# Kernel tuning notes

Measured on AMD Instinct MI355X. Metric: run time of the kernel, lower is better.

Reference implementation:

```python
import jax, jax.numpy as jnp
import numpy as np

K_NEIGHBORS = 16


def knn_idx(x, k):
    # x: (bs, n, 3) -> (bs, n, k) indices of k nearest points (incl. self)
    sq = jnp.sum(x * x, axis=-1)                      # (bs, n)
    inner = jnp.einsum('bnd,bmd->bnm', x, x)          # (bs, n, n)
    dist = sq[:, :, None] - 2.0 * inner + sq[:, None, :]
    _, idx = jax.lax.top_k(-dist, k)
    return idx


def gather_neighbors(feat, idx):
    # feat: (bs, n, d), idx: (bs, n, k) -> (bs, n, k, d)
    bs = feat.shape[0]
    return feat[jnp.arange(bs)[:, None, None], idx]


def setup_inputs() -> dict:
    key = jax.random.key(0)
    ks = jax.random.split(key, 20)
    bs, n, emb, inner, ph, ah = 4, 2048, 128, 128, 64, 4 * 128
    s = lambda k, sh, fan: jax.random.normal(k, sh, jnp.float32) * (1.0 / np.sqrt(fan))
    return {
        'query': jax.random.normal(ks[0], (bs, n, emb), jnp.float32),
        'key': jax.random.normal(ks[1], (bs, n, emb), jnp.float32),
        'value': jax.random.normal(ks[2], (bs, n, emb), jnp.float32),
        'canonical': jax.random.normal(ks[3], (bs, n, 3), jnp.float32),
        'wq': s(ks[4], (emb, inner), emb),
        'wk': s(ks[5], (emb, inner), emb),
        'wv': s(ks[6], (emb, inner), emb),
        'wo': s(ks[7], (inner, emb), inner),
        'bo': jnp.zeros((emb,), jnp.float32),
        'p1': s(ks[8], (3, ph), 3),
        'pb1': jnp.zeros((ph,), jnp.float32),
        'p2': s(ks[9], (ph, inner), ph),
        'pb2': jnp.zeros((inner,), jnp.float32),
        'a1': s(ks[10], (inner, ah), inner),
        'ab1': jnp.zeros((ah,), jnp.float32),
        'a2': s(ks[11], (ah, inner), ah),
        'ab2': jnp.zeros((inner,), jnp.float32),
    }


def reference(query, key, value, canonical, wq, wk, wv, wo, bo,
              p1, pb1, p2, pb2, a1, ab1, a2, ab2):
    k_nb = K_NEIGHBORS
    q = query @ wq                                    # (bs, n, d)
    k = key @ wk
    v = value @ wv
    idx = knn_idx(canonical, k_nb)                    # (bs, n, k)

    pos_nn = gather_neighbors(canonical, idx)         # (bs, n, k, 3)
    rel_pos = pos_nn - canonical[:, :, None, :]
    rel_pos_emb = jax.nn.relu(rel_pos @ p1 + pb1) @ p2 + pb2  # (bs, n, k, d)

    q_nn = gather_neighbors(q, idx)
    k_nn = gather_neighbors(k, idx)
    v_nn = gather_neighbors(v, idx) + rel_pos_emb

    sim = jax.nn.relu((q_nn - k_nn + rel_pos_emb) @ a1 + ab1) @ a2 + ab2
    attn = jax.nn.softmax(sim, axis=-1)               # softmax over feature dim
    norm = jnp.maximum(jnp.linalg.norm(attn, axis=-2, keepdims=True), 1e-12)
    attn = attn / norm                                # L2-normalize over neighbors

    agg = jnp.einsum('bijd,bijd->bid', attn, v_nn)    # (bs, n, d)
    return agg @ wo + bo
```

## Files before the change

kernel.cpp:

```cpp
#include <hip/hip_runtime.h>
#include <stdint.h>

typedef unsigned short u16;
typedef unsigned int u32;
typedef unsigned long long u64;
typedef __attribute__((ext_vector_type(8))) short short8;
typedef __attribute__((ext_vector_type(4))) float f32x4;

#define BSZ 4
#define NPT 2048
#define EMB 128
#define PH  64
#define AH  512
#define KNB 16

__device__ __forceinline__ u16 f2bf(float f) {
  union { float f; u32 u; } v; v.f = f;
  u32 r = (v.u >> 16) & 1u;
  v.u += 0x7fffu + r;
  return (u16)(v.u >> 16);
}
__device__ __forceinline__ float bf2f(u16 x) {
  union { u32 u; float f; } v; v.u = ((u32)x) << 16; return v.f;
}

__global__ __launch_bounds__(256) void k_transpose(
    const float* wq, const float* wk, const float* wv, const float* p2,
    const float* a1, const float* a2, const float* wo,
    u16* wqT, u16* wkT, u16* wvT, u16* p2T, u16* a1T, u16* a2T, u16* woT) {
  const float* src; u16* dst; int K, Nn;
  switch (blockIdx.x) {
    case 0: src = wq; dst = wqT; K = 128; Nn = 128; break;
    case 1: src = wk; dst = wkT; K = 128; Nn = 128; break;
    case 2: src = wv; dst = wvT; K = 128; Nn = 128; break;
    case 3: src = p2; dst = p2T; K = 64;  Nn = 128; break;
    case 4: src = a1; dst = a1T; K = 128; Nn = 512; break;
    case 5: src = a2; dst = a2T; K = 512; Nn = 128; break;
    default: src = wo; dst = woT; K = 128; Nn = 128; break;
  }
  for (int n = threadIdx.x; n < Nn; n += 256) {
    for (int k0 = 0; k0 < K; k0 += 8) {
      short8 vv;
      #pragma unroll
      for (int t = 0; t < 8; ++t)
        vv[t] = (short)f2bf(src[(k0 + t) * Nn + n]);
      *(short8*)(dst + n * K + k0) = vv;
    }
  }
}

__device__ __forceinline__ u32 f2sort(float f) {
  union { float f; u32 u; } v; v.f = f;
  return v.u ^ ((v.u >> 31) ? 0xFFFFFFFFu : 0x80000000u);
}

__global__ __launch_bounds__(256) void k_knn(const float* __restrict__ can,
                                             int* __restrict__ idx_out) {
  __shared__ float dists[4][NPT];
  int b = blockIdx.x >> 8;
  int qblk = blockIdx.x & 255;
  const float* cb = can + (size_t)b * NPT * 3;
  int wave = threadIdx.x >> 6, lane = threadIdx.x & 63;
  float* dw = dists[wave];
  #pragma unroll 1
  for (int t = 0; t < 2; ++t) {
    int i = qblk * 8 + wave * 2 + t;
    float xi = cb[i * 3 + 0], yi = cb[i * 3 + 1], zi = cb[i * 3 + 2];
    float sqi = __fadd_rn(__fadd_rn(__fmul_rn(xi, xi), __fmul_rn(yi, yi)),
                          __fmul_rn(zi, zi));
    u64 lmin = ~0ull;
    #pragma unroll 4
    for (int c = 0; c < NPT / 64; ++c) {
      int j = c * 64 + lane;
      const float* pj = cb + j * 3;
      float xj = pj[0], yj = pj[1], zj = pj[2];
      float sqj = __fadd_rn(__fadd_rn(__fmul_rn(xj, xj), __fmul_rn(yj, yj)),
                            __fmul_rn(zj, zj));
      float nn = __fadd_rn(__fadd_rn(__fmul_rn(xi, xj), __fmul_rn(yi, yj)),
                           __fmul_rn(zi, zj));
      float dist = __fadd_rn(__fsub_rn(sqi, __fmul_rn(2.0f, nn)), sqj);
      dw[j] = dist;
      u64 key = (((u64)f2sort(dist)) << 32) | (u32)j;
      lmin = key < lmin ? key : lmin;
    }
    #pragma unroll 1
    for (int r = 0; r < KNB; ++r) {
      u64 g = lmin;
      #pragma unroll
      for (int off = 32; off > 0; off >>= 1) {
        u64 o = __shfl_xor(g, off);
        g = o < g ? o : g;
      }
      int jw = (int)(u32)(g & 0xffffffffull);
      if (lane == 0) idx_out[((size_t)b * NPT + i) * KNB + r] = jw;
      if ((jw & 63) == lane) {
        union { u32 u; float f; } inf; inf.u = 0x7f800000u;
        dw[jw] = inf.f;
        lmin = ~0ull;
        #pragma unroll
        for (int c = 0; c < NPT / 64; ++c) {
          int j = c * 64 + lane;
          u64 key = (((u64)f2sort(dw[j])) << 32) | (u32)j;
          lmin = key < lmin ? key : lmin;
        }
      }
    }
  }
}

__device__ __forceinline__ void qkv_gemm(const u16* At, const u16* wT,
                                         int colbase, int fm, int quad,
                                         f32x4 acc[2][4]) {
  #pragma unroll
  for (int tn = 0; tn < 2; ++tn)
    #pragma unroll
    for (int tm = 0; tm < 4; ++tm) acc[tn][tm] = (f32x4){0.f, 0.f, 0.f, 0.f};
  #pragma unroll
  for (int ks = 0; ks < 4; ++ks) {
    int k0 = ks * 32 + quad * 8;
    short8 bfr0 = *(const short8*)(wT + (colbase + fm) * 128 + k0);
    short8 bfr1 = *(const short8*)(wT + (colbase + 16 + fm) * 128 + k0);
    #pragma unroll
    for (int tm = 0; tm < 4; ++tm) {
      short8 afr = *(const short8*)(At + (tm * 16 + fm) * 136 + k0);
      acc[0][tm] = __builtin_amdgcn_mfma_f32_16x16x32_bf16(afr, bfr0, acc[0][tm], 0, 0, 0);
      acc[1][tm] = __builtin_amdgcn_mfma_f32_16x16x32_bf16(afr, bfr1, acc[1][tm], 0, 0, 0);
    }
  }
}

__device__ __forceinline__ void qkv_stage(u16* At, const float* src, int rbase, int tid) {
  #pragma unroll
  for (int rep = 0; rep < 4; ++rep) {
    int linear = tid + 256 * rep;
    int row = linear >> 4;
    int c16 = linear & 15;
    const float* sp = src + (size_t)(rbase + row) * 128 + c16 * 8;
    f32x4 a = *(const f32x4*)(sp);
    f32x4 b = *(const f32x4*)(sp + 4);
    short8 vv;
    vv[0] = (short)f2bf(a[0]); vv[1] = (short)f2bf(a[1]);
    vv[2] = (short)f2bf(a[2]); vv[3] = (short)f2bf(a[3]);
    vv[4] = (short)f2bf(b[0]); vv[5] = (short)f2bf(b[1]);
    vv[6] = (short)f2bf(b[2]); vv[7] = (short)f2bf(b[3]);
    *(short8*)(At + row * 136 + c16 * 8) = vv;
  }
}

__global__ __launch_bounds__(256) void k_qkv(
    const float* __restrict__ query, const float* __restrict__ key,
    const float* __restrict__ value,
    const u16* __restrict__ wqT, const u16* __restrict__ wkT,
    const u16* __restrict__ wvT,
    u32* __restrict__ pv_out) {
  __shared__ __align__(16) u16 At[64 * 136];
  int tid = threadIdx.x;
  int rbase = blockIdx.x * 64;
  int lane = tid & 63, wave = tid >> 6;
  int fm = lane & 15, quad = lane >> 4;
  int colbase = wave * 32;
  f32x4 accq[2][4], acck[2][4];

  qkv_stage(At, query, rbase, tid);
  __syncthreads();
  qkv_gemm(At, wqT, colbase, fm, quad, accq);
  __syncthreads();
  qkv_stage(At, key, rbase, tid);
  __syncthreads();
  qkv_gemm(At, wkT, colbase, fm, quad, acck);
  u32 qk2[4][4];
  #pragma unroll
  for (int tm = 0; tm < 4; ++tm)
    #pragma unroll
    for (int r = 0; r < 4; ++r)
      qk2[tm][r] = (u32)f2bf(accq[0][tm][r] - acck[0][tm][r]) |
                   (((u32)f2bf(accq[1][tm][r] - acck[1][tm][r])) << 16);
  __syncthreads();
  qkv_stage(At, value, rbase, tid);
  __syncthreads();
  qkv_gemm(At, wvT, colbase, fm, quad, accq);
  #pragma unroll
  for (int tn = 0; tn < 2; ++tn) {
    int col = colbase + tn * 16 + fm;
    #pragma unroll
    for (int tm = 0; tm < 4; ++tm)
      #pragma unroll
      for (int r = 0; r < 4; ++r) {
        int row = tm * 16 + quad * 4 + r;
        u32 qkb = tn == 0 ? (qk2[tm][r] & 0xffffu) : (qk2[tm][r] >> 16);
        u32 pack = qkb | (((u32)f2bf(accq[tn][tm][r])) << 16);
        pv_out[(size_t)(rbase + row) * 128 + col] = pack;
      }
  }
}

#define XT_LD 136

__global__ __launch_bounds__(256, 3) void k_attn(
    const float* __restrict__ can,
    const u32* __restrict__ pv_g,
    const int* __restrict__ idx_g,
    const float* __restrict__ p1, const float* __restrict__ pb1,
    const u16* __restrict__ p2T, const float* __restrict__ pb2,
    const u16* __restrict__ a1T, const float* __restrict__ ab1,
    const u16* __restrict__ a2T, const float* __restrict__ ab2,
    const u16* __restrict__ woT, const float* __restrict__ bo,
    float* __restrict__ out) {
  __shared__ __align__(16) char smem[39168];
  u16* Xt = (u16*)(smem);
  u16* Hs = (u16*)(smem + 17408);
  u16* R1 = (u16*)(smem + 17408);
  float* Red1 = (float*)(smem + 34816);
  float* Red2 = (float*)(smem + 35840);
  float* Agg = (float*)(smem + 36864);
  int* Idx = (int*)(smem + 38912);

  const int b = blockIdx.x >> 9;
  const int qbase = (blockIdx.x & 511) * 4;
  const int tid = threadIdx.x;
  const int lane = tid & 63, wave = tid >> 6;
  const int fm = lane & 15, quad = lane >> 4;
  const int colbase = wave * 32;

  if (tid < 64) Idx[tid] = idx_g[((size_t)b * NPT + qbase) * KNB + tid];
  __syncthreads();

  u32 pvld[2][4][4];
  #pragma unroll
  for (int tn = 0; tn < 2; ++tn) {
    int col = colbase + tn * 16 + fm;
    #pragma unroll
    for (int tm = 0; tm < 4; ++tm)
      #pragma unroll
      for (int r = 0; r < 4; ++r) {
        int row = tm * 16 + quad * 4 + r;
        int j = Idx[row];
        pvld[tn][tm][r] = pv_g[((size_t)b * NPT + j) * EMB + col];
      }
  }

  {
    int row = tid >> 2, part = tid & 3;
    int j = Idx[row];
    int qi = qbase + (row >> 4);
    const float* cb = can + (size_t)b * NPT * 3;
    float r0 = cb[j * 3 + 0] - cb[qi * 3 + 0];
    float r1 = cb[j * 3 + 1] - cb[qi * 3 + 1];
    float r2 = cb[j * 3 + 2] - cb[qi * 3 + 2];
    #pragma unroll
    for (int hp = 0; hp < 8; ++hp) {
      int cp = part + 4 * hp;
      u32 pack = 0;
      #pragma unroll
      for (int e = 0; e < 2; ++e) {
        int hh = cp * 2 + e;
        float s = r0 * p1[hh];
        s = fmaf(r1, p1[PH + hh], s);
        s = fmaf(r2, p1[2 * PH + hh], s);
        s += pb1[hh];
        s = fmaxf(s, 0.0f);
        pack |= ((u32)f2bf(s)) << (16 * e);
      }
      *(u32*)(R1 + row * 72 + cp * 2) = pack;
    }
  }
  __syncthreads();

  u32 vp[4][4];
  {
    f32x4 acc[2][4];
    #pragma unroll
    for (int tn = 0; tn < 2; ++tn)
      #pragma unroll
      for (int tm = 0; tm < 4; ++tm) acc[tn][tm] = (f32x4){0.f, 0.f, 0.f, 0.f};
    #pragma unroll
    for (int ks = 0; ks < 2; ++ks) {
      int k0 = ks * 32 + quad * 8;
      short8 bfr0 = *(const short8*)(p2T + (colbase + fm) * PH + k0);
      short8 bfr1 = *(const short8*)(p2T + (colbase + 16 + fm) * PH + k0);
      #pragma unroll
      for (int tm = 0; tm < 4; ++tm) {
        short8 afr = *(const short8*)(R1 + (tm * 16 + fm) * 72 + k0);
        acc[0][tm] = __builtin_amdgcn_mfma_f32_16x16x32_bf16(afr, bfr0, acc[0][tm], 0, 0, 0);
        acc[1][tm] = __builtin_amdgcn_mfma_f32_16x16x32_bf16(afr, bfr1, acc[1][tm], 0, 0, 0);
      }
    }
    #pragma unroll
    for (int tn = 0; tn < 2; ++tn) {
      int col = colbase + tn * 16 + fm;
      float pb2c = pb2[col];
      #pragma unroll
      for (int tm = 0; tm < 4; ++tm)
        #pragma unroll
        for (int r = 0; r < 4; ++r) {
          int row = tm * 16 + quad * 4 + r;
          float rpe = acc[tn][tm][r] + pb2c;
          u32 w = pvld[tn][tm][r];
          Xt[row * XT_LD + col] = f2bf(bf2f((u16)(w & 0xffffu)) + rpe);
          u32 vb = (u32)f2bf(bf2f((u16)(w >> 16)) + rpe);
          if (tn == 0) vp[tm][r] = vb; else vp[tm][r] |= vb << 16;
        }
    }
  }
  __syncthreads();

  f32x4 accS[2][4];
  #pragma unroll
  for (int tn = 0; tn < 2; ++tn)
    #pragma unroll
    for (int tm = 0; tm < 4; ++tm) accS[tn][tm] = (f32x4){0.f, 0.f, 0.f, 0.f};
  #pragma unroll 1
  for (int c = 0; c < 4; ++c) {
    f32x4 acc1[2][4];
    #pragma unroll
    for (int tn = 0; tn < 2; ++tn)
      #pragma unroll
      for (int tm = 0; tm < 4; ++tm) acc1[tn][tm] = (f32x4){0.f, 0.f, 0.f, 0.f};
    #pragma unroll
    for (int ks = 0; ks < 4; ++ks) {
      int k0 = ks * 32 + quad * 8;
      short8 bfr0 = *(const short8*)(a1T + (c * 128 + colbase + fm) * 128 + k0);
      short8 bfr1 = *(const short8*)(a1T + (c * 128 + colbase + 16 + fm) * 128 + k0);
      #pragma unroll
      for (int tm = 0; tm < 4; ++tm) {
        short8 afr = *(const short8*)(Xt + (tm * 16 + fm) * XT_LD + k0);
        acc1[0][tm] = __builtin_amdgcn_mfma_f32_16x16x32_bf16(afr, bfr0, acc1[0][tm], 0, 0, 0);
        acc1[1][tm] = __builtin_amdgcn_mfma_f32_16x16x32_bf16(afr, bfr1, acc1[1][tm], 0, 0, 0);
      }
    }
    #pragma unroll
    for (int tn = 0; tn < 2; ++tn) {
      int lcol = colbase + tn * 16 + fm;
      float ab1c = ab1[c * 128 + lcol];
      #pragma unroll
      for (int tm = 0; tm < 4; ++tm)
        #pragma unroll
        for (int r = 0; r < 4; ++r) {
          int row = tm * 16 + quad * 4 + r;
          Hs[row * XT_LD + lcol] = f2bf(fmaxf(acc1[tn][tm][r] + ab1c, 0.0f));
        }
    }
    __syncthreads();
    #pragma unroll
    for (int ks = 0; ks < 4; ++ks) {
      int k0 = ks * 32 + quad * 8;
      short8 bfr0 = *(const short8*)(a2T + (colbase + fm) * AH + c * 128 + k0);
      short8 bfr1 = *(const short8*)(a2T + (colbase + 16 + fm) * AH + c * 128 + k0);
      #pragma unroll
      for (int tm = 0; tm < 4; ++tm) {
        short8 afr = *(const short8*)(Hs + (tm * 16 + fm) * XT_LD + k0);
        accS[0][tm] = __builtin_amdgcn_mfma_f32_16x16x32_bf16(afr, bfr0, accS[0][tm], 0, 0, 0);
        accS[1][tm] = __builtin_amdgcn_mfma_f32_16x16x32_bf16(afr, bfr1, accS[1][tm], 0, 0, 0);
      }
    }
    __syncthreads();
  }

  {
    float ab2c0 = ab2[colbase + fm];
    float ab2c1 = ab2[colbase + 16 + fm];
    float rm[4][4];
    #pragma unroll
    for (int tm = 0; tm < 4; ++tm)
      #pragma unroll
      for (int r = 0; r < 4; ++r) {
        accS[0][tm][r] += ab2c0;
        accS[1][tm][r] += ab2c1;
        rm[tm][r] = fmaxf(accS[0][tm][r], accS[1][tm][r]);
      }
    #pragma unroll
    for (int off = 1; off <= 8; off <<= 1)
      #pragma unroll
      for (int tm = 0; tm < 4; ++tm)
        #pragma unroll
        for (int r = 0; r < 4; ++r)
          rm[tm][r] = fmaxf(rm[tm][r], __shfl_xor(rm[tm][r], off));
    if (fm == 0) {
      #pragma unroll
      for (int tm = 0; tm < 4; ++tm)
        #pragma unroll
        for (int r = 0; r < 4; ++r)
          Red1[wave * 64 + tm * 16 + quad * 4 + r] = rm[tm][r];
    }
    __syncthreads();
    #pragma unroll
    for (int tm = 0; tm < 4; ++tm)
      #pragma unroll
      for (int r = 0; r < 4; ++r) {
        int row = tm * 16 + quad * 4 + r;
        float m = fmaxf(fmaxf(Red1[row], Red1[64 + row]),
                        fmaxf(Red1[128 + row], Red1[192 + row]));
        float e0 = __expf(accS[0][tm][r] - m);
        float e1 = __expf(accS[1][tm][r] - m);
        accS[0][tm][r] = e0;
        accS[1][tm][r] = e1;
        rm[tm][r] = e0 + e1;
      }
    #pragma unroll
    for (int off = 1; off <= 8; off <<= 1)
      #pragma unroll
      for (int tm = 0; tm < 4; ++tm)
        #pragma unroll
        for (int r = 0; r < 4; ++r)
          rm[tm][r] += __shfl_xor(rm[tm][r], off);
    if (fm == 0) {
      #pragma unroll
      for (int tm = 0; tm < 4; ++tm)
        #pragma unroll
        for (int r = 0; r < 4; ++r)
          Red2[wave * 64 + tm * 16 + quad * 4 + r] = rm[tm][r];
    }
    __syncthreads();
    #pragma unroll
    for (int tm = 0; tm < 4; ++tm)
      #pragma unroll
      for (int r = 0; r < 4; ++r) {
        int row = tm * 16 + quad * 4 + r;
        float sum = (Red2[row] + Red2[64 + row]) +
                    (Red2[128 + row] + Red2[192 + row]);
        float inv = 1.0f / sum;
        accS[0][tm][r] *= inv;
        accS[1][tm][r] *= inv;
      }
  }

  #pragma unroll
  for (int tn = 0; tn < 2; ++tn)
    #pragma unroll
    for (int tm = 0; tm < 4; ++tm) {
      float ssq = 0.f, wav = 0.f;
      #pragma unroll
      for (int r = 0; r < 4; ++r) {
        float a = accS[tn][tm][r];
        u16 vb = (u16)(tn == 0 ? (vp[tm][r] & 0xffffu) : (vp[tm][r] >> 16));
        ssq = fmaf(a, a, ssq);
        wav = fmaf(a, bf2f(vb), wav);
      }
      ssq += __shfl_xor(ssq, 16); ssq += __shfl_xor(ssq, 32);
      wav += __shfl_xor(wav, 16); wav += __shfl_xor(wav, 32);
      if (quad == 0)
        Agg[tm * EMB + colbase + tn * 16 + fm] =
            wav / fmaxf(sqrtf(ssq), 1e-12f);
    }
  __syncthreads();

  {
    int d = tid & 127, qp = tid >> 7;
    float boc = bo[d];
    #pragma unroll
    for (int qi2 = 0; qi2 < 2; ++qi2) {
      int q = qp * 2 + qi2;
      float o = 0.f;
      #pragma unroll
      for (int k8 = 0; k8 < 16; ++k8) {
        short8 w8 = *(const short8*)(woT + d * 128 + k8 * 8);
        #pragma unroll
        for (int e = 0; e < 8; ++e)
          o = fmaf(Agg[q * EMB + k8 * 8 + e], bf2f((u16)w8[e]), o);
      }
      out[((size_t)b * NPT + qbase + q) * EMB + d] = o + boc;
    }
  }
}

extern "C" void kernel_launch(void* const* d_in, const int* in_sizes, int n_in,
                              void* d_out, int out_size, void* d_ws, size_t ws_size,
                              hipStream_t stream) {
  (void)in_sizes; (void)n_in; (void)out_size; (void)ws_size;
  const float* query = (const float*)d_in[0];
  const float* key_i = (const float*)d_in[1];
  const float* value = (const float*)d_in[2];
  const float* can   = (const float*)d_in[3];
  const float* wq  = (const float*)d_in[4];
  const float* wk  = (const float*)d_in[5];
  const float* wv  = (const float*)d_in[6];
  const float* wo  = (const float*)d_in[7];
  const float* bo  = (const float*)d_in[8];
  const float* p1  = (const float*)d_in[9];
  const float* pb1 = (const float*)d_in[10];
  const float* p2  = (const float*)d_in[11];
  const float* pb2 = (const float*)d_in[12];
  const float* a1  = (const float*)d_in[13];
  const float* ab1 = (const float*)d_in[14];
  const float* a2  = (const float*)d_in[15];
  const float* ab2 = (const float*)d_in[16];

  char* ws = (char*)d_ws;
  u32* pv_ws = (u32*)(ws + 0);
  int* idx_ws  = (int*)(ws + 8388608);
  u16* wqT = (u16*)(ws + 8912896);
  u16* wkT = (u16*)(ws + 8945664);
  u16* wvT = (u16*)(ws + 8978432);
  u16* p2T = (u16*)(ws + 9011200);
  u16* a1T = (u16*)(ws + 9027584);
  u16* a2T = (u16*)(ws + 9158656);
  u16* woT = (u16*)(ws + 9289728);
  float* out = (float*)d_out;

  k_transpose<<<dim3(7), dim3(256), 0, stream>>>(
      wq, wk, wv, p2, a1, a2, wo, wqT, wkT, wvT, p2T, a1T, a2T, woT);
  k_knn<<<dim3(1024), dim3(256), 0, stream>>>(can, idx_ws);
  k_qkv<<<dim3(128), dim3(256), 0, stream>>>(
      query, key_i, value, wqT, wkT, wvT, pv_ws);
  k_attn<<<dim3(2048), dim3(256), 0, stream>>>(
      can, pv_ws, idx_ws, p1, pb1, p2T, pb2, a1T, ab1, a2T, ab2,
      woT, bo, out);
}
```

Baseline: 319.1 us.

## Give each wave one query's neighbor rows so softmax and MLP need no block syncs

The attention kernel's MFMA work is repartitioned from a column split (each wave owning 32 of 128 feature columns across all 64 neighbor rows) to a row split (each wave owning the 16 neighbor rows of one query across all 128 columns). Softmax over the feature dimension then reduces within a wave using shuffles, so the shared-memory max/sum reduction buffers and most __syncthreads barriers in the MLP chunk loop are dropped. Each wave now reads all B-fragments of a1/a2/p2 instead of a quarter of them, which raises weight-load traffic from L1/L2, while A-fragment reuse per wave falls. Shared memory shrinks slightly.

```diff
diff --git a/kernel.cpp b/kernel.cpp
--- a/kernel.cpp
+++ b/kernel.cpp
@@ -206,43 +206,39 @@
     const u16* __restrict__ a2T, const float* __restrict__ ab2,
     const u16* __restrict__ woT, const float* __restrict__ bo,
     float* __restrict__ out) {
-  __shared__ __align__(16) char smem[39168];
+  __shared__ __align__(16) char smem[37120];
   u16* Xt = (u16*)(smem);
   u16* Hs = (u16*)(smem + 17408);
   u16* R1 = (u16*)(smem + 17408);
-  float* Red1 = (float*)(smem + 34816);
-  float* Red2 = (float*)(smem + 35840);
-  float* Agg = (float*)(smem + 36864);
-  int* Idx = (int*)(smem + 38912);
+  float* Agg = (float*)(smem + 34816);
+  int* Idx = (int*)(smem + 36864);
 
   const int b = blockIdx.x >> 9;
   const int qbase = (blockIdx.x & 511) * 4;
   const int tid = threadIdx.x;
-  const int lane = tid & 63, wave = tid >> 6;
+  const int lane = tid & 63, w = tid >> 6;
   const int fm = lane & 15, quad = lane >> 4;
-  const int colbase = wave * 32;
 
   if (tid < 64) Idx[tid] = idx_g[((size_t)b * NPT + qbase) * KNB + tid];
   __syncthreads();
 
-  u32 pvld[2][4][4];
-  #pragma unroll
-  for (int tn = 0; tn < 2; ++tn) {
-    int col = colbase + tn * 16 + fm;
-    #pragma unroll
-    for (int tm = 0; tm < 4; ++tm)
-      #pragma unroll
-      for (int r = 0; r < 4; ++r) {
-        int row = tm * 16 + quad * 4 + r;
-        int j = Idx[row];
-        pvld[tn][tm][r] = pv_g[((size_t)b * NPT + j) * EMB + col];
-      }
+  int jreg[4];
+  #pragma unroll
+  for (int r = 0; r < 4; ++r) jreg[r] = Idx[w * 16 + quad * 4 + r];
+
+  u32 pvld[8][4];
+  #pragma unroll
+  for (int tn = 0; tn < 8; ++tn) {
+    int col = tn * 16 + fm;
+    #pragma unroll
+    for (int r = 0; r < 4; ++r)
+      pvld[tn][r] = pv_g[((size_t)b * NPT + jreg[r]) * EMB + col];
   }
 
   {
-    int row = tid >> 2, part = tid & 3;
-    int j = Idx[row];
-    int qi = qbase + (row >> 4);
+    int lrow = lane >> 2, part = lane & 3;
+    int j = Idx[w * 16 + lrow];
+    int qi = qbase + w;
     const float* cb = can + (size_t)b * NPT * 3;
     float r0 = cb[j * 3 + 0] - cb[qi * 3 + 0];
     float r1 = cb[j * 3 + 1] - cb[qi * 3 + 1];
@@ -261,187 +257,142 @@
         s = fmaxf(s, 0.0f);
         pack |= ((u32)f2bf(s)) << (16 * e);
       }
-      *(u32*)(R1 + row * 72 + cp * 2) = pack;
-    }
-  }
-  __syncthreads();
+      *(u32*)(R1 + (w * 16 + lrow) * 72 + cp * 2) = pack;
+    }
+  }
 
   u32 vp[4][4];
   {
-    f32x4 acc[2][4];
-    #pragma unroll
-    for (int tn = 0; tn < 2; ++tn)
-      #pragma unroll
-      for (int tm = 0; tm < 4; ++tm) acc[tn][tm] = (f32x4){0.f, 0.f, 0.f, 0.f};
+    f32x4 acc[8];
+    #pragma unroll
+    for (int tn = 0; tn < 8; ++tn) acc[tn] = (f32x4){0.f, 0.f, 0.f, 0.f};
     #pragma unroll
     for (int ks = 0; ks < 2; ++ks) {
       int k0 = ks * 32 + quad * 8;
-      short8 bfr0 = *(const short8*)(p2T + (colbase + fm) * PH + k0);
-      short8 bfr1 = *(const short8*)(p2T + (colbase + 16 + fm) * PH + k0);
-      #pragma unroll
-      for (int tm = 0; tm < 4; ++tm) {
-        short8 afr = *(const short8*)(R1 + (tm * 16 + fm) * 72 + k0);
-        acc[0][tm] = __builtin_amdgcn_mfma_f32_16x16x32_bf16(afr, bfr0, acc[0][tm], 0, 0, 0);
-        acc[1][tm] = __builtin_amdgcn_mfma_f32_16x16x32_bf16(afr, bfr1, acc[1][tm], 0, 0, 0);
-      }
-    }
-    #pragma unroll
-    for (int tn = 0; tn < 2; ++tn) {
-      int col = colbase + tn * 16 + fm;
+      short8 afr = *(const short8*)(R1 + (w * 16 + fm) * 72 + k0);
+      #pragma unroll
+      for (int tn = 0; tn < 8; ++tn) {
+        short8 bfr = *(const short8*)(p2T + (tn * 16 + fm) * PH + k0);
+        acc[tn] = __builtin_amdgcn_mfma_f32_16x16x32_bf16(afr, bfr, acc[tn], 0, 0, 0);
+      }
+    }
+    #pragma unroll
+    for (int tn = 0; tn < 8; ++tn) {
+      int col = tn * 16 + fm;
       float pb2c = pb2[col];
       #pragma unroll
-      for (int tm = 0; tm < 4; ++tm)
-        #pragma unroll
-        for (int r = 0; r < 4; ++r) {
-          int row = tm * 16 + quad * 4 + r;
-          float rpe = acc[tn][tm][r] + pb2c;
-          u32 w = pvld[tn][tm][r];
-          Xt[row * XT_LD + col] = f2bf(bf2f((u16)(w & 0xffffu)) + rpe);
-          u32 vb = (u32)f2bf(bf2f((u16)(w >> 16)) + rpe);
-          if (tn == 0) vp[tm][r] = vb; else vp[tm][r] |= vb << 16;
-        }
-    }
-  }
-  __syncthreads();
-
-  f32x4 accS[2][4];
-  #pragma unroll
-  for (int tn = 0; tn < 2; ++tn)
-    #pragma unroll
-    for (int tm = 0; tm < 4; ++tm) accS[tn][tm] = (f32x4){0.f, 0.f, 0.f, 0.f};
+      for (int r = 0; r < 4; ++r) {
+        int row = w * 16 + quad * 4 + r;
+        float rpe = acc[tn][r] + pb2c;
+        u32 wv2 = pvld[tn][r];
+        Xt[row * XT_LD + col] = f2bf(bf2f((u16)(wv2 & 0xffffu)) + rpe);
+        u32 vb = (u32)f2bf(bf2f((u16)(wv2 >> 16)) + rpe);
+        if ((tn & 1) == 0) vp[tn >> 1][r] = vb;
+        else vp[tn >> 1][r] |= vb << 16;
+      }
+    }
+  }
+
+  f32x4 accS[8];
+  #pragma unroll
+  for (int tn = 0; tn < 8; ++tn) accS[tn] = (f32x4){0.f, 0.f, 0.f, 0.f};
   #pragma unroll 1
   for (int c = 0; c < 4; ++c) {
-    f32x4 acc1[2][4];
-    #pragma unroll
-    for (int tn = 0; tn < 2; ++tn)
-      #pragma unroll
-      for (int tm = 0; tm < 4; ++tm) acc1[tn][tm] = (f32x4){0.f, 0.f, 0.f, 0.f};
+    f32x4 acc1[8];
+    #pragma unroll
+    for (int tn = 0; tn < 8; ++tn) acc1[tn] = (f32x4){0.f, 0.f, 0.f, 0.f};
     #pragma unroll
     for (int ks = 0; ks < 4; ++ks) {
       int k0 = ks * 32 + quad * 8;
-      short8 bfr0 = *(const short8*)(a1T + (c * 128 + colbase + fm) * 128 + k0);
-      short8 bfr1 = *(const short8*)(a1T + (c * 128 + colbase + 16 + fm) * 128 + k0);
-      #pragma unroll
-      for (int tm = 0; tm < 4; ++tm) {
-        short8 afr = *(const short8*)(Xt + (tm * 16 + fm) * XT_LD + k0);
-        acc1[0][tm] = __builtin_amdgcn_mfma_f32_16x16x32_bf16(afr, bfr0, acc1[0][tm], 0, 0, 0);
-        acc1[1][tm] = __builtin_amdgcn_mfma_f32_16x16x32_bf16(afr, bfr1, acc1[1][tm], 0, 0, 0);
-      }
-    }
-    #pragma unroll
-    for (int tn = 0; tn < 2; ++tn) {
-      int lcol = colbase + tn * 16 + fm;
+      short8 afr = *(const short8*)(Xt + (w * 16 + fm) * XT_LD + k0);
+      #pragma unroll
+      for (int tn = 0; tn < 8; ++tn) {
+        short8 bfr = *(const short8*)(a1T + (c * 128 + tn * 16 + fm) * 128 + k0);
+        acc1[tn] = __builtin_amdgcn_mfma_f32_16x16x32_bf16(afr, bfr, acc1[tn], 0, 0, 0);
+      }
+    }
+    #pragma unroll
+    for (int tn = 0; tn < 8; ++tn) {
+      int lcol = tn * 16 + fm;
       float ab1c = ab1[c * 128 + lcol];
       #pragma unroll
-      for (int tm = 0; tm < 4; ++tm)
-        #pragma unroll
-        for (int r = 0; r < 4; ++r) {
-          int row = tm * 16 + quad * 4 + r;
-          Hs[row * XT_LD + lcol] = f2bf(fmaxf(acc1[tn][tm][r] + ab1c, 0.0f));
-        }
-    }
-    __syncthreads();
+      for (int r = 0; r < 4; ++r) {
+        int row = w * 16 + quad * 4 + r;
+        Hs[row * XT_LD + lcol] = f2bf(fmaxf(acc1[tn][r] + ab1c, 0.0f));
+      }
+    }
     #pragma unroll
     for (int ks = 0; ks < 4; ++ks) {
       int k0 = ks * 32 + quad * 8;
-      short8 bfr0 = *(const short8*)(a2T + (colbase + fm) * AH + c * 128 + k0);
-      short8 bfr1 = *(const short8*)(a2T + (colbase + 16 + fm) * AH + c * 128 + k0);
-      #pragma unroll
-      for (int tm = 0; tm < 4; ++tm) {
-        short8 afr = *(const short8*)(Hs + (tm * 16 + fm) * XT_LD + k0);
-        accS[0][tm] = __builtin_amdgcn_mfma_f32_16x16x32_bf16(afr, bfr0, accS[0][tm], 0, 0, 0);
-        accS[1][tm] = __builtin_amdgcn_mfma_f32_16x16x32_bf16(afr, bfr1, accS[1][tm], 0, 0, 0);
-      }
-    }
-    __syncthreads();
+      short8 afr = *(const short8*)(Hs + (w * 16 + fm) * XT_LD + k0);
+      #pragma unroll
+      for (int tn = 0; tn < 8; ++tn) {
+        short8 bfr = *(const short8*)(a2T + (tn * 16 + fm) * AH + c * 128 + k0);
+        accS[tn] = __builtin_amdgcn_mfma_f32_16x16x32_bf16(afr, bfr, accS[tn], 0, 0, 0);
+      }
+    }
   }
 
   {
-    float ab2c0 = ab2[colbase + fm];
-    float ab2c1 = ab2[colbase + 16 + fm];
-    float rm[4][4];
-    #pragma unroll
-    for (int tm = 0; tm < 4; ++tm)
-      #pragma unroll
-      for (int r = 0; r < 4; ++r) {
-        accS[0][tm][r] += ab2c0;
-        accS[1][tm][r] += ab2c1;
-        rm[tm][r] = fmaxf(accS[0][tm][r], accS[1][tm][r]);
-      }
+    float ab2c[8];
+    #pragma unroll
+    for (int tn = 0; tn < 8; ++tn) ab2c[tn] = ab2[tn * 16 + fm];
+    float rm[4], sm[4];
+    #pragma unroll
+    for (int r = 0; r < 4; ++r) {
+      float m = accS[0][r] + ab2c[0];
+      #pragma unroll
+      for (int tn = 0; tn < 8; ++tn) {
+        accS[tn][r] += ab2c[tn];
+        m = fmaxf(m, accS[tn][r]);
+      }
+      rm[r] = m;
+    }
     #pragma unroll
     for (int off = 1; off <= 8; off <<= 1)
       #pragma unroll
-      for (int tm = 0; tm < 4; ++tm)
-        #pragma unroll
-        for (int r = 0; r < 4; ++r)
-          rm[tm][r] = fmaxf(rm[tm][r], __shfl_xor(rm[tm][r], off));
-    if (fm == 0) {
-      #pragma unroll
-      for (int tm = 0; tm < 4; ++tm)
-        #pragma unroll
-        for (int r = 0; r < 4; ++r)
-          Red1[wave * 64 + tm * 16 + quad * 4 + r] = rm[tm][r];
-    }
-    __syncthreads();
-    #pragma unroll
-    for (int tm = 0; tm < 4; ++tm)
-      #pragma unroll
-      for (int r = 0; r < 4; ++r) {
-        int row = tm * 16 + quad * 4 + r;
-        float m = fmaxf(fmaxf(Red1[row], Red1[64 + row]),
-                        fmaxf(Red1[128 + row], Red1[192 + row]));
-        float e0 = __expf(accS[0][tm][r] - m);
-        float e1 = __expf(accS[1][tm][r] - m);
-        accS[0][tm][r] = e0;
-        accS[1][tm][r] = e1;
-        rm[tm][r] = e0 + e1;
-      }
+      for (int r = 0; r < 4; ++r)
+        rm[r] = fmaxf(rm[r], __shfl_xor(rm[r], off));
+    #pragma unroll
+    for (int r = 0; r < 4; ++r) {
+      float s = 0.f;
+      #pragma unroll
+      for (int tn = 0; tn < 8; ++tn) {
+        float e = __expf(accS[tn][r] - rm[r]);
+        accS[tn][r] = e;
+        s += e;
+      }
+      sm[r] = s;
+    }
     #pragma unroll
     for (int off = 1; off <= 8; off <<= 1)
       #pragma unroll
-      for (int tm = 0; tm < 4; ++tm)
-        #pragma unroll
-        for (int r = 0; r < 4; ++r)
-          rm[tm][r] += __shfl_xor(rm[tm][r], off);
-    if (fm == 0) {
-      #pragma unroll
-      for (int tm = 0; tm < 4; ++tm)
-        #pragma unroll
-        for (int r = 0; r < 4; ++r)
-          Red2[wave * 64 + tm * 16 + quad * 4 + r] = rm[tm][r];
-    }
-    __syncthreads();
-    #pragma unroll
-    for (int tm = 0; tm < 4; ++tm)
-      #pragma unroll
-      for (int r = 0; r < 4; ++r) {
-        int row = tm * 16 + quad * 4 + r;
-        float sum = (Red2[row] + Red2[64 + row]) +
-                    (Red2[128 + row] + Red2[192 + row]);
-        float inv = 1.0f / sum;
-        accS[0][tm][r] *= inv;
-        accS[1][tm][r] *= inv;
-      }
-  }
-
-  #pragma unroll
-  for (int tn = 0; tn < 2; ++tn)
-    #pragma unroll
-    for (int tm = 0; tm < 4; ++tm) {
-      float ssq = 0.f, wav = 0.f;
-      #pragma unroll
-      for (int r = 0; r < 4; ++r) {
-        float a = accS[tn][tm][r];
-        u16 vb = (u16)(tn == 0 ? (vp[tm][r] & 0xffffu) : (vp[tm][r] >> 16));
-        ssq = fmaf(a, a, ssq);
-        wav = fmaf(a, bf2f(vb), wav);
-      }
-      ssq += __shfl_xor(ssq, 16); ssq += __shfl_xor(ssq, 32);
-      wav += __shfl_xor(wav, 16); wav += __shfl_xor(wav, 32);
-      if (quad == 0)
-        Agg[tm * EMB + colbase + tn * 16 + fm] =
-            wav / fmaxf(sqrtf(ssq), 1e-12f);
-    }
+      for (int r = 0; r < 4; ++r)
+        sm[r] += __shfl_xor(sm[r], off);
+    #pragma unroll
+    for (int r = 0; r < 4; ++r) {
+      float inv = 1.0f / sm[r];
+      #pragma unroll
+      for (int tn = 0; tn < 8; ++tn) accS[tn][r] *= inv;
+    }
+  }
+
+  #pragma unroll
+  for (int tn = 0; tn < 8; ++tn) {
+    float ssq = 0.f, wav = 0.f;
+    #pragma unroll
+    for (int r = 0; r < 4; ++r) {
+      float a = accS[tn][r];
+      u16 vb = (u16)((tn & 1) == 0 ? (vp[tn >> 1][r] & 0xffffu)
+                                   : (vp[tn >> 1][r] >> 16));
+      ssq = fmaf(a, a, ssq);
+      wav = fmaf(a, bf2f(vb), wav);
+    }
+    ssq += __shfl_xor(ssq, 16); ssq += __shfl_xor(ssq, 32);
+    wav += __shfl_xor(wav, 16); wav += __shfl_xor(wav, 32);
+    if (quad == 0)
+      Agg[w * EMB + tn * 16 + fm] = wav / fmaxf(sqrtf(ssq), 1e-12f);
+  }
   __syncthreads();
 
   {
```

New measurement: 490.7 us. 53.7% more time.

## Double-buffer hidden activations and prefetch MLP weight fragments into registers

Applied to the files above, without the earlier changes.

Adds two alternating shared-memory buffers for the hidden activations so the trailing barrier in each chunk loop can be dropped. The a1 and a2 weight fragments are loaded into registers ahead of use, with the next chunk's a1 fragments fetched before the barrier so their latency overlaps. This raises shared memory per block to about 54 KB and adds register pressure, which may lower occupancy below the declared 3 blocks per CU.

```diff
diff --git a/kernel.cpp b/kernel.cpp
--- a/kernel.cpp
+++ b/kernel.cpp
@@ -206,14 +206,12 @@
     const u16* __restrict__ a2T, const float* __restrict__ ab2,
     const u16* __restrict__ woT, const float* __restrict__ bo,
     float* __restrict__ out) {
-  __shared__ __align__(16) char smem[39168];
+  __shared__ __align__(16) char smem[54528];
   u16* Xt = (u16*)(smem);
-  u16* Hs = (u16*)(smem + 17408);
-  u16* R1 = (u16*)(smem + 17408);
-  float* Red1 = (float*)(smem + 34816);
-  float* Red2 = (float*)(smem + 35840);
-  float* Agg = (float*)(smem + 36864);
-  int* Idx = (int*)(smem + 38912);
+  float* Red1 = (float*)(smem);
+  float* Red2 = (float*)(smem + 1024);
+  float* Agg = (float*)(smem + 52224);
+  int* Idx = (int*)(smem + 54272);
 
   const int b = blockIdx.x >> 9;
   const int qbase = (blockIdx.x & 511) * 4;
@@ -239,6 +237,7 @@
       }
   }
 
+  u16* R1 = (u16*)(smem + 17408);
   {
     int row = tid >> 2, part = tid & 3;
     int j = Idx[row];
@@ -304,6 +303,13 @@
   }
   __syncthreads();
 
+  short8 a1f[4][2], a2f[4][2];
+  #pragma unroll
+  for (int ks = 0; ks < 4; ++ks) {
+    int k0 = ks * 32 + quad * 8;
+    a1f[ks][0] = *(const short8*)(a1T + (colbase + fm) * 128 + k0);
+    a1f[ks][1] = *(const short8*)(a1T + (colbase + 16 + fm) * 128 + k0);
+  }
   f32x4 accS[2][4];
   #pragma unroll
   for (int tn = 0; tn < 2; ++tn)
@@ -311,6 +317,7 @@
     for (int tm = 0; tm < 4; ++tm) accS[tn][tm] = (f32x4){0.f, 0.f, 0.f, 0.f};
   #pragma unroll 1
   for (int c = 0; c < 4; ++c) {
+    u16* HsB = (u16*)(smem + 17408 + (c & 1) * 17408);
     f32x4 acc1[2][4];
     #pragma unroll
     for (int tn = 0; tn < 2; ++tn)
@@ -319,13 +326,11 @@
     #pragma unroll
     for (int ks = 0; ks < 4; ++ks) {
       int k0 = ks * 32 + quad * 8;
-      short8 bfr0 = *(const short8*)(a1T + (c * 128 + colbase + fm) * 128 + k0);
-      short8 bfr1 = *(const short8*)(a1T + (c * 128 + colbase + 16 + fm) * 128 + k0);
       #pragma unroll
       for (int tm = 0; tm < 4; ++tm) {
         short8 afr = *(const short8*)(Xt + (tm * 16 + fm) * XT_LD + k0);
-        acc1[0][tm] = __builtin_amdgcn_mfma_f32_16x16x32_bf16(afr, bfr0, acc1[0][tm], 0, 0, 0);
-        acc1[1][tm] = __builtin_amdgcn_mfma_f32_16x16x32_bf16(afr, bfr1, acc1[1][tm], 0, 0, 0);
+        acc1[0][tm] = __builtin_amdgcn_mfma_f32_16x16x32_bf16(afr, a1f[ks][0], acc1[0][tm], 0, 0, 0);
+        acc1[1][tm] = __builtin_amdgcn_mfma_f32_16x16x32_bf16(afr, a1f[ks][1], acc1[1][tm], 0, 0, 0);
       }
     }
     #pragma unroll
@@ -337,23 +342,34 @@
         #pragma unroll
         for (int r = 0; r < 4; ++r) {
           int row = tm * 16 + quad * 4 + r;
-          Hs[row * XT_LD + lcol] = f2bf(fmaxf(acc1[tn][tm][r] + ab1c, 0.0f));
+          HsB[row * XT_LD + lcol] = f2bf(fmaxf(acc1[tn][tm][r] + ab1c, 0.0f));
         }
     }
-    __syncthreads();
     #pragma unroll
     for (int ks = 0; ks < 4; ++ks) {
       int k0 = ks * 32 + quad * 8;
-      short8 bfr0 = *(const short8*)(a2T + (colbase + fm) * AH + c * 128 + k0);
-      short8 bfr1 = *(const short8*)(a2T + (colbase + 16 + fm) * AH + c * 128 + k0);
+      a2f[ks][0] = *(const short8*)(a2T + (colbase + fm) * AH + c * 128 + k0);
+      a2f[ks][1] = *(const short8*)(a2T + (colbase + 16 + fm) * AH + c * 128 + k0);
+    }
+    if (c < 3) {
+      #pragma unroll
+      for (int ks = 0; ks < 4; ++ks) {
+        int k0 = ks * 32 + quad * 8;
+        a1f[ks][0] = *(const short8*)(a1T + ((c + 1) * 128 + colbase + fm) * 128 + k0);
+        a1f[ks][1] = *(const short8*)(a1T + ((c + 1) * 128 + colbase + 16 + fm) * 128 + k0);
+      }
+    }
+    __syncthreads();
+    #pragma unroll
+    for (int ks = 0; ks < 4; ++ks) {
+      int k0 = ks * 32 + quad * 8;
       #pragma unroll
       for (int tm = 0; tm < 4; ++tm) {
-        short8 afr = *(const short8*)(Hs + (tm * 16 + fm) * XT_LD + k0);
-        accS[0][tm] = __builtin_amdgcn_mfma_f32_16x16x32_bf16(afr, bfr0, accS[0][tm], 0, 0, 0);
-        accS[1][tm] = __builtin_amdgcn_mfma_f32_16x16x32_bf16(afr, bfr1, accS[1][tm], 0, 0, 0);
-      }
-    }
-    __syncthreads();
+        short8 afr = *(const short8*)(HsB + (tm * 16 + fm) * XT_LD + k0);
+        accS[0][tm] = __builtin_amdgcn_mfma_f32_16x16x32_bf16(afr, a2f[ks][0], accS[0][tm], 0, 0, 0);
+        accS[1][tm] = __builtin_amdgcn_mfma_f32_16x16x32_bf16(afr, a2f[ks][1], accS[1][tm], 0, 0, 0);
+      }
+    }
   }
 
   {
```

Measured after the change: 344.7 us. 8.0% more time.
